# Kernel optimization log

Measured on AMD Instinct MI355X. Metric: run time of the kernel, lower is better.

The kernel has to match this reference:

```python
import jax, jax.numpy as jnp
import numpy as np
import math

B, C, H, W_ = 64, 1024, 10, 10      # C = vis_chans = ir_chans = lan_chans = m_chans
NTOK, MTOK = H * W_, 20             # 100 image tokens (W1: 100x100), 20 text tokens (W2: 100x20)
K_NN, BIG, EPS = 8, 1.0e6, 1e-8


def _minmax(t):
    # per-sample min-max normalization over the full distance slice
    mn = t.min(axis=(1, 2), keepdims=True)
    mx = t.max(axis=(1, 2), keepdims=True)
    return (t - mn) / (mx - mn + EPS)


def _geodesic(X):
    # Isomap-style geodesic distances: symmetric 8-NN Euclidean graph + Floyd-Warshall.
    P = X.shape[0]
    sq = jnp.sum(X * X, axis=-1)
    D = jnp.sqrt(jnp.maximum(sq[:, None] + sq[None, :] - 2.0 * (X @ X.T), 0.0))
    Dm = D + jnp.eye(P, dtype=X.dtype) * BIG          # exclude self from kNN
    negd, idx = jax.lax.top_k(-Dm, K_NN)              # 8 nearest neighbors per node
    A = jnp.full((P, P), BIG, X.dtype).at[jnp.arange(P)[:, None], idx].set(-negd)
    Wg = jnp.minimum(A, A.T)                          # undirected graph
    Wg = Wg.at[jnp.diag_indices(P)].set(0.0)

    def body(Dk, k):
        return jnp.minimum(Dk, Dk[:, k][:, None] + Dk[k, :][None, :]), None

    Wg, _ = jax.lax.scan(body, Wg, jnp.arange(P))
    return Wg


def _forward(ir, vis, lan, vis_w, vis_b, vis_g, vis_be, ir_w, ir_b, ir_g, ir_be,
             t_w, t_b, vout_w, vout_b, tout_w, tout_b, W1, b1, W2, b2, W4, W5,
             ml_w, ml_b, ml2_w, ml2_b, scalars):
    lam1, lam2, a1, be1, g1, a2, be2, g2, wg_aw, wg_ab, wg_bw, wg_bb = scalars
    sqc = jnp.sqrt(jnp.float32(C))
    vis_r = vis.reshape(B, C, -1).transpose(0, 2, 1)   # [B,100,C]
    ir_r = ir.reshape(B, C, -1).transpose(0, 2, 1)     # [B,100,C]
    lan_t = lan.transpose(0, 2, 1)                     # [B,20,C]

    geo = jax.vmap(_geodesic)

    # ---- compute_M_image (detached in original) ----
    joint_vi = jnp.concatenate([vis_r, ir_r], axis=1)                    # [B,200,C]
    d_vi = jax.lax.stop_gradient(geo(joint_vi))[:, :NTOK, NTOK:]         # [B,100,100]
    M_v2i_dist = _minmax(d_vi)
    sigma = jax.lax.stop_gradient(jnp.median(M_v2i_dist))
    M_v2i_fix = jnp.exp(-M_v2i_dist ** 2 / (2.0 * sigma ** 2))
    lam1s = jax.nn.sigmoid(lam1)
    M_v2i_learn = lam1s * M_v2i_fix + (1.0 - lam1s) * (W1 * M_v2i_fix + b1)

    def conv_in_relu(x, w3, b3, g3, be3, i):
        # 1x1 conv + InstanceNorm2d(affine) + ReLU, flattened to tokens
        y = jnp.einsum('bchw,mc->bmhw', x, w3[i]) + b3[i][None, :, None, None]
        mu = y.mean((2, 3), keepdims=True)
        var = y.var((2, 3), keepdims=True)
        y = (y - mu) / jnp.sqrt(var + 1e-5) * g3[i][None, :, None, None] + be3[i][None, :, None, None]
        return jax.nn.relu(y).reshape(B, C, -1).transpose(0, 2, 1)       # [B,100,C]

    Qv, Kv, Vv = [conv_in_relu(vis, vis_w, vis_b, vis_g, vis_be, i) for i in range(3)]
    Qi, Ki, Vi = [conv_in_relu(ir, ir_w, ir_b, ir_g, ir_be, i) for i in range(3)]
    Qt, Kt, Vt = [jax.nn.relu(lan_t @ t_w[i].T + t_b[i]) for i in range(3)]

    # fusion weights from GAP of the learned manifold matrix
    Mgap = M_v2i_learn.mean((1, 2), keepdims=True)       # [B,1,1]
    alpha = jax.nn.sigmoid(wg_aw * Mgap + wg_ab)
    beta = jax.nn.sigmoid(wg_bw * Mgap + wg_bb)
    Qf, Kf, Vf = alpha * Qv + beta * Qi, alpha * Kv + beta * Ki, alpha * Vv + beta * Vi
    feat_img = alpha * vis_r + beta * ir_r               # [B,100,C]

    # ---- compute_M_text (detached in original) ----
    joint_it = jnp.concatenate([feat_img, lan_t], axis=1)                # [B,120,C]
    d_it = jax.lax.stop_gradient(geo(joint_it))
    M_i2t_dist = _minmax(d_it[:, :NTOK, NTOK:])          # [B,100,20] (unused downstream, as in original)
    M_t2i_dist = _minmax(d_it[:, NTOK:, :NTOK])          # [B,20,100]
    sigma2 = jax.lax.stop_gradient(jnp.median(M_t2i_dist))
    M_t2i_fix = jnp.exp(-M_t2i_dist ** 2 / (2.0 * sigma2 ** 2))          # [B,20,100]
    M_i2t_fix = M_t2i_fix.transpose(0, 2, 1)                             # [B,100,20]
    lam2s = jax.nn.sigmoid(lam2)
    M_i2t_lo = lam2s * M_i2t_fix + (1.0 - lam2s) * (W2 * M_i2t_fix + b2) # [B,100,20]
    M_t2i_lo = M_i2t_lo.transpose(0, 2, 1)                               # [B,20,100]
    M_t2i_lo = jax.nn.softmax(M_t2i_lo / sqc, axis=2)
    M_i2t_lo = jax.nn.softmax(M_i2t_lo / sqc, axis=2)
    M_t2i_learn = (M_i2t_lo @ lan_t) @ ml_w.T + ml_b       # [B,100,C]
    M_i2t_learn = (M_t2i_lo @ feat_img) @ ml2_w.T + ml2_b  # [B,20,C]

    # ---- text->image cross attention ----
    A = Qt @ Kf.transpose(0, 2, 1) \
        + a1 * (Qt @ M_t2i_learn.transpose(0, 2, 1)) \
        + be1 * (W4 @ (M_t2i_learn @ Kf.transpose(0, 2, 1)))
    Av = jax.nn.softmax(A / sqc, axis=2)                   # [B,20,100]
    new_lan = Av @ Vf + g1 * (M_t2i_lo @ Vf)               # [B,20,C]

    # ---- image->text cross attention ----
    Bm = Qf @ Kt.transpose(0, 2, 1) \
        + a2 * (Qf @ M_i2t_learn.transpose(0, 2, 1)) \
        + be2 * (W5 @ (M_i2t_learn @ Kt.transpose(0, 2, 1)))
    Bv = jax.nn.softmax(Bm / sqc, axis=2)                  # [B,100,20]
    new_vis = Bv @ Vt + g2 * (M_i2t_lo @ Vt)               # [B,100,C]

    new_vis = new_vis.transpose(0, 2, 1).reshape(B, C, H, W_)
    new_vis = jnp.einsum('bchw,mc->bmhw', new_vis, vout_w) + vout_b[None, :, None, None]
    new_lan = new_lan @ tout_w.T + tout_b

    # ---- regularization loss ----
    fA = jax.nn.softmax(M_t2i_fix / sqc, axis=2)
    fB = jax.nn.softmax(M_i2t_fix / sqc, axis=2)
    l1 = jnp.abs(Av - fA).mean() + jnp.abs(Bv - fB).mean()
    var = lambda x: jnp.var(x, ddof=1)                    # torch .var() is unbiased
    l2 = -jnp.abs(var(Av) - var(fA)) - jnp.abs(var(Bv) - var(fB))
    loss = (l1 + 100.0 * l2) * 1000.0
    return new_vis, new_lan, loss


def setup_inputs() -> dict:
    key = jax.random.key(0)
    ks = jax.random.split(key, 20)
    f = lambda k, s, sc=1.0: jax.random.normal(k, s, jnp.float32) * sc
    return dict(
        ir=f(ks[0], (B, C, H, W_)),
        vis=f(ks[1], (B, C, H, W_)),
        lan=f(ks[2], (B, C, MTOK)),
        vis_w=f(ks[3], (3, C, C), 0.02), vis_b=jnp.zeros((3, C), jnp.float32),
        vis_g=jnp.ones((3, C), jnp.float32), vis_be=jnp.zeros((3, C), jnp.float32),
        ir_w=f(ks[4], (3, C, C), 0.02), ir_b=jnp.zeros((3, C), jnp.float32),
        ir_g=jnp.ones((3, C), jnp.float32), ir_be=jnp.zeros((3, C), jnp.float32),
        t_w=f(ks[5], (3, C, C), 0.02), t_b=jnp.zeros((3, C), jnp.float32),
        vout_w=f(ks[6], (C, C), 0.02), vout_b=jnp.zeros((C,), jnp.float32),
        tout_w=f(ks[7], (C, C), 0.02), tout_b=jnp.zeros((C,), jnp.float32),
        W1=f(ks[8], (NTOK, NTOK), 0.1), b1=jnp.zeros((NTOK, NTOK), jnp.float32),
        W2=f(ks[9], (NTOK, MTOK), 0.1), b2=jnp.zeros((NTOK, MTOK), jnp.float32),
        W4=f(ks[10], (MTOK, NTOK), 0.1),
        W5=f(ks[11], (NTOK, MTOK), 0.1),
        ml_w=f(ks[12], (C, C), 0.02), ml_b=jnp.zeros((C,), jnp.float32),
        ml2_w=f(ks[13], (C, C), 0.02), ml2_b=jnp.zeros((C,), jnp.float32),
        # [lam1, lam2, a1, b1, g1, a2, b2, g2, wg_aw, wg_ab, wg_bw, wg_bb]
        scalars=jnp.array([0.5, 0.5, 0.5, 0.5, 0.5, 0.5, 0.5, 0.5, 0.3, 0.0, 0.3, 0.0], jnp.float32),
    )


def reference(ir, vis, lan, vis_w, vis_b, vis_g, vis_be, ir_w, ir_b, ir_g, ir_be,
              t_w, t_b, vout_w, vout_b, tout_w, tout_b, W1, b1, W2, b2, W4, W5,
              ml_w, ml_b, ml2_w, ml2_b, scalars):
    return _forward(ir, vis, lan, vis_w, vis_b, vis_g, vis_be, ir_w, ir_b, ir_g, ir_be,
                    t_w, t_b, vout_w, vout_b, tout_w, tout_b, W1, b1, W2, b2, W4, W5,
                    ml_w, ml_b, ml2_w, ml2_b, scalars)
```

## Files before the change

kernel.cpp:

```cpp
#include <hip/hip_runtime.h>
#include <hip/hip_bf16.h>
#include <math.h>

#define B_   64
#define C_   1024
#define HW   100
#define MT_  20
#define P1   200
#define P2   120
#define BIGF 1.0e6f
#define EPSF 1e-8f
#define SQC  32.0f

static constexpr size_t F_J    = 0;
static constexpr size_t N_J    = (size_t)B_*P1*C_;
static constexpr size_t F_D    = F_J + N_J;
static constexpr size_t N_D    = (size_t)B_*P1*P1;
static constexpr size_t F_SQ   = F_D + N_D;
static constexpr size_t N_SQ   = (size_t)B_*P1;
static constexpr size_t F_KNN  = F_SQ + N_SQ;
static constexpr size_t N_KNN  = (size_t)B_*P1*8;
static constexpr size_t F_MV   = F_KNN + N_KNN;
static constexpr size_t N_MV   = (size_t)B_*HW*HW;
static constexpr size_t F_MT   = F_MV + N_MV;
// ... 41 lines not shown
  int c0 = blockIdx.x*32, p0 = blockIdx.y*32, b = blockIdx.z;
  int j = threadIdx.x & 31, i0 = threadIdx.x >> 5;
  for (int i = i0; i < 32; i += 8){
    int p = p0 + j;
    float v = 0.f;
    if (p < P1) v = (p < HW) ? vis[((size_t)b*C_ + c0+i)*HW + p]
                             : ir [((size_t)b*C_ + c0+i)*HW + (p-HW)];
    tile[i][j] = v;
  }
  __syncthreads();
  for (int i = i0; i < 32; i += 8){
    int p = p0 + i;
    if (p < P1) J[((size_t)b*P1 + p)*C_ + c0 + j] = tile[j][i];
  }
}

__global__ void k_pack_j2(const float* __restrict__ feat, const float* __restrict__ lan,
                          float* __restrict__ J){
  int idx = blockIdx.x*256 + threadIdx.x;
  if (idx >= B_*P2*C_) return;
  int c = idx & (C_-1);
  int p = (idx >> 10) % P2;
  int b = idx / (C_*P2);
  float v;
  if (p < HW) v = feat[((size_t)b*HW + p)*C_ + c];
  else        v = lan [((size_t)b*C_ + c)*MT_ + (p-HW)];
  J[idx] = v;
}

__global__ void k_rowsq(const float* __restrict__ J, float* __restrict__ sq, int P){
  int row = blockIdx.x;
  const float* r = J + (size_t)row*C_;
  float s = 0.f;
  for (int c = threadIdx.x; c < C_; c += 64){ float v = r[c]; s += v*v; }
  for (int o = 32; o > 0; o >>= 1) s += __shfl_down(s, o);
  if (threadIdx.x == 0) sq[row] = s;
}

__global__ __launch_bounds__(256) void k_gram_dist(const float* __restrict__ J,
    const float* __restrict__ sq, float* __restrict__ D, int P){
  __shared__ float Xi[64][33], Xj[64][33];
  int b = blockIdx.z;
  int r0 = blockIdx.x*64, s0 = blockIdx.y*64;
  int tx = threadIdx.x & 15, ty = threadIdx.x >> 4;
  const float* Jb = J + (size_t)b*P*C_;
  float acc[4][4];
  #pragma unroll
  for (int u = 0; u < 4; u++)
    #pragma unroll
    for (int v = 0; v < 4; v++) acc[u][v] = 0.f;
  for (int c0 = 0; c0 < C_; c0 += 32){
    for (int e = threadIdx.x; e < 2048; e += 256){
      int rr = e >> 5, cc = e & 31;
      Xi[rr][cc] = (r0+rr < P) ? Jb[(size_t)(r0+rr)*C_ + c0+cc] : 0.f;
      Xj[rr][cc] = (s0+rr < P) ? Jb[(size_t)(s0+rr)*C_ + c0+cc] : 0.f;
    }
    __syncthreads();
    for (int kk = 0; kk < 32; kk++){
      float xr[4], xs[4];
      #pragma unroll
      for (int u = 0; u < 4; u++) xr[u] = Xi[ty*4+u][kk];
      #pragma unroll
      for (int v = 0; v < 4; v++) xs[v] = Xj[tx*4+v][kk];
      #pragma unroll
      for (int u = 0; u < 4; u++)
        #pragma unroll
        for (int v = 0; v < 4; v++) acc[u][v] += xr[u]*xs[v];
    }
    __syncthreads();
  }
  #pragma unroll
  for (int u = 0; u < 4; u++){
    #pragma unroll
    for (int v = 0; v < 4; v++){
      int r = r0 + ty*4 + u, s = s0 + tx*4 + v;
      if (r < P && s < P){
        float d2 = sq[b*P+r] + sq[b*P+s] - 2.f*acc[u][v];
        D[((size_t)b*P + r)*P + s] = sqrtf(fmaxf(d2, 0.f));
      }
    }
  }
}

template<int P>
__global__ void k_knn(const float* __restrict__ D, int* __restrict__ knn){
  constexpr int NS = (P + 63)/64;
  int row = blockIdx.x;
  int i = row % P;
  const float* Dr = D + (size_t)row*P;
  float v[NS];
  #pragma unroll
  for (int t = 0; t < NS; t++){
    int j = threadIdx.x + t*64;
    float d = (j < P) ? Dr[j] : 4.0e6f;
    if (j == i) d += BIGF;
    v[t] = d;
  }
  for (int k = 0; k < 8; k++){
    float bv = 3.4e38f; int bj = 1 << 30;
    #pragma unroll
    for (int t = 0; t < NS; t++){
      int j = threadIdx.x + t*64;
      if (v[t] < bv){ bv = v[t]; bj = j; }
    }
    for (int o = 32; o > 0; o >>= 1){
      float ov = __shfl_xor(bv, o);
      int   oj = __shfl_xor(bj, o);
      if (ov < bv || (ov == bv && oj < bj)){ bv = ov; bj = oj; }
    }
    if (threadIdx.x == 0) knn[(size_t)row*8 + k] = bj;
    if ((bj & 63) == (int)threadIdx.x){
      #pragma unroll
      for (int t = 0; t < NS; t++) if (t == (bj >> 6)) v[t] = 3.9e38f;
    }
  }
}

__global__ void k_buildw(float* __restrict__ D, const int* __restrict__ knn, int P){
  int idx = blockIdx.x*256 + threadIdx.x;
  if (idx >= B_*P*P) return;
  int s = idx % P; int r = (idx/P) % P; int b = idx/(P*P);
  float w;
  if (r == s) w = 0.f;
  else {
    const int* ki = knn + ((size_t)b*P + r)*8;
    const int* kj = knn + ((size_t)b*P + s)*8;
    bool e = false;
    #pragma unroll
    for (int k = 0; k < 8; k++) e = e || (ki[k] == s) || (kj[k] == r);
    w = e ? D[idx] : BIGF;
  }
  D[idx] = w;
}

template<int P, int RP, int CP>
__global__ __launch_bounds__(1024) void k_fw(float* __restrict__ D){
  constexpr int PR = P/RP;
  constexpr int PC = P/CP;
  constexpr int NTH = PR*PC;
  __shared__ float rowk[P], colk[P];
  float* Db = D + (size_t)blockIdx.x*P*P;
  int tid = threadIdx.x;
  bool act = tid < NTH;
  int pi = tid / PC, pj = tid - pi*PC;
  int i0 = pi*RP, j0 = pj*CP;
  float w[RP][CP];
  if (act){
    #pragma unroll
    for (int r = 0; r < RP; r++){
      float4 v = *(const float4*)(Db + (size_t)(i0+r)*P + j0);
      w[r][0]=v.x; w[r][1]=v.y; w[r][2]=v.z; w[r][3]=v.w;
    }
  }
  for (int k = 0; k < P; k++){
    if (act){
      #pragma unroll
      for (int r = 0; r < RP; r++){
        if (i0 + r == k)
          *(float4*)(rowk + j0) = make_float4(w[r][0],w[r][1],w[r][2],w[r][3]);
      }
      #pragma unroll
      for (int c = 0; c < CP; c++){
        if (j0 + c == k){
          #pragma unroll
          for (int r = 0; r < RP; r++) colk[i0+r] = w[r][c];
        }
      }
    }
    __syncthreads();
    if (act){
      float4 rk4 = *(const float4*)(rowk + j0);
      float rk[4] = {rk4.x, rk4.y, rk4.z, rk4.w};
      float ck[RP];
      #pragma unroll
      for (int r = 0; r < RP; r++) ck[r] = colk[i0+r];
      #pragma unroll
      for (int r = 0; r < RP; r++)
        #pragma unroll
        for (int c = 0; c < CP; c++)
          w[r][c] = fminf(w[r][c], ck[r] + rk[c]);
    }
    __syncthreads();
  }
  if (act){
    #pragma unroll
    for (int r = 0; r < RP; r++)
      *(float4*)(Db + (size_t)(i0+r)*P + j0) = make_float4(w[r][0],w[r][1],w[r][2],w[r][3]);
  }
}

__global__ __launch_bounds__(256) void k_minmax(const float* __restrict__ D,
    float* __restrict__ out, int P, int r0, int c0, int R, int Cc){
  __shared__ float smn[256], smx[256];
  int b = blockIdx.x;
  const float* Db = D + (size_t)b*P*P;
  float mn = 3.4e38f, mx = -3.4e38f;
  for (int e = threadIdx.x; e < R*Cc; e += 256){
    int i = e / Cc, j = e - i*Cc;
    float v = Db[(size_t)(r0+i)*P + c0+j];
    mn = fminf(mn, v); mx = fmaxf(mx, v);
  }
  smn[threadIdx.x] = mn; smx[threadIdx.x] = mx;
  __syncthreads();
  for (int o = 128; o > 0; o >>= 1){
    if ((int)threadIdx.x < o){
      smn[threadIdx.x] = fminf(smn[threadIdx.x], smn[threadIdx.x+o]);
      smx[threadIdx.x] = fmaxf(smx[threadIdx.x], smx[threadIdx.x+o]);
    }
    __syncthreads();
  }
  mn = smn[0]; mx = smx[0];
  float inv = 1.f/(mx - mn + EPSF);
  for (int e = threadIdx.x; e < R*Cc; e += 256){
    int i = e / Cc, j = e - i*Cc;
    float v = Db[(size_t)(r0+i)*P + c0+j];
    out[((size_t)b*R + i)*Cc + j] = (v - mn)*inv;
  }
}

__global__ void k_med_init(float* hs){ if (threadIdx.x == 0){ hs[0] = 0.f; hs[1] = 1.0f; } }

__global__ __launch_bounds__(256) void k_med_hist(const float* __restrict__ x, int N,
                           const float* __restrict__ hs, unsigned* __restrict__ hist){
  __shared__ unsigned lh[1025];
  for (int i = threadIdx.x; i < 1025; i += 256) lh[i] = 0u;
  __syncthreads();
  float lo = hs[0], hi = hs[1];
  float scale = 1024.f/(hi - lo);
  unsigned below = 0;
  int idx = blockIdx.x*256 + threadIdx.x;
  int stride = gridDim.x*256;
  for (int i = idx; i < N; i += stride){
    float v = x[i];
    if (v < lo) below++;
    else if (v < hi){
      int bn = (int)((v - lo)*scale);
      if (bn > 1023) bn = 1023;
      atomicAdd(&lh[bn], 1u);
    }
  }
  for (int o = 32; o > 0; o >>= 1) below += __shfl_down(below, o);
  if ((threadIdx.x & 63) == 0 && below) atomicAdd(&lh[1024], below);
  __syncthreads();
  for (int i = threadIdx.x; i < 1025; i += 256){
    unsigned v = lh[i];
    if (v) atomicAdd(&hist[i], v);
  }
}

__global__ void k_med_select(float* hs, const unsigned* __restrict__ hist, int k){
  if (threadIdx.x != 0) return;
  float lo = hs[0], hi = hs[1], w = (hi - lo)*(1.f/1024.f);
  unsigned cum = hist[1024];
  int bf = 1023;
  for (int bn = 0; bn < 1024; bn++){
    unsigned h = hist[bn];
    if (cum + h > (unsigned)k){ bf = bn; break; }
    cum += h;
  }
  hs[0] = lo + bf*w; hs[1] = lo + (bf+1)*w;
}

__global__ __launch_bounds__(256) void k_mgap(const float* __restrict__ Mv,
    const float* __restrict__ W1, const float* __restrict__ b1,
    const float* __restrict__ sc, const float* __restrict__ hs,
    float* __restrict__ alpha, float* __restrict__ bet){
  __shared__ float sr[256];
  int b = blockIdx.x;
  float lam1s = 1.f/(1.f + expf(-sc[0]));
  float sig = 0.5f*(hs[0] + hs[1]);
  float inv2s = 1.f/(2.f*sig*sig);
  const float* Mb = Mv + (size_t)b*HW*HW;
  float s = 0.f;
  for (int e = threadIdx.x; e < HW*HW; e += 256){
    float v = Mb[e];
    float f = expf(-v*v*inv2s);
    s += lam1s*f + (1.f - lam1s)*(W1[e]*f + b1[e]);
  }
  sr[threadIdx.x] = s; __syncthreads();
  for (int o = 128; o > 0; o >>= 1){
    if ((int)threadIdx.x < o) sr[threadIdx.x] += sr[threadIdx.x+o];
    __syncthreads();
  }
  if (threadIdx.x == 0){
    float mg = sr[0]*(1.f/(HW*HW));
    alpha[b] = 1.f/(1.f + expf(-(sc[8]*mg + sc[9])));
    bet[b]   = 1.f/(1.f + expf(-(sc[10]*mg + sc[11])));
  }
}

__global__ void k_castw(const float* __restrict__ a, const float* __restrict__ b,
                        short* __restrict__ oa, short* __restrict__ ob){
  int i = (blockIdx.x*256 + threadIdx.x)*4;
  if (i >= 3*C_*C_) return;
  float4 va = *(const float4*)(a + i);
  float4 vb = *(const float4*)(b + i);
  short ra[4] = { f2bf(va.x), f2bf(va.y), f2bf(va.z), f2bf(va.w) };
  short rb[4] = { f2bf(vb.x), f2bf(vb.y), f2bf(vb.z), f2bf(vb.w) };
  *(bhalf*)(oa + i) = *(bhalf*)ra;
  *(bhalf*)(ob + i) = *(bhalf*)rb;
}

__global__ void k_cast(const float* __restrict__ a, short* __restrict__ oa, int n){
  int i = (blockIdx.x*256 + threadIdx.x)*4;
  if (i >= n) return;
  float4 va = *(const float4*)(a + i);
  short ra[4] = { f2bf(va.x), f2bf(va.y), f2bf(va.z), f2bf(va.w) };
  *(bhalf*)(oa + i) = *(bhalf*)ra;
}

__global__ __launch_bounds__(256) void k_xt2(const float* __restrict__ V,
    const float* __restrict__ I, short* __restrict__ XtV, short* __restrict__ XtI){
  __shared__ float tv[32][33], ti[32][33];
  int c0 = blockIdx.x*32, t0 = blockIdx.y*32, b = blockIdx.z;
  int j = threadIdx.x & 31, i0 = threadIdx.x >> 5;
  for (int i = i0; i < 32; i += 8){
    int t = t0 + j;
    float a = 0.f, c = 0.f;
    if (t < HW){
      a = V[((size_t)b*C_ + c0+i)*HW + t];
      c = I[((size_t)b*C_ + c0+i)*HW + t];
    }
    tv[i][j] = a; ti[i][j] = c;
  }
  __syncthreads();
  for (int i = i0; i < 32; i += 8){
    int t = t0 + i;
    if (t < HW){
      XtV[((size_t)b*HW + t)*C_ + c0 + j] = f2bf(tv[j][i]);
      XtI[((size_t)b*HW + t)*C_ + c0 + j] = f2bf(ti[j][i]);
    }
  }
}

__global__ __launch_bounds__(256) void k_lanT(const float* __restrict__ lan,
                                              short* __restrict__ lanT){
  __shared__ float tile[32][21];
  int c0 = blockIdx.x*32, b = blockIdx.y;
  for (int e = threadIdx.x; e < 32*MT_; e += 256){
    int c = e / MT_, t = e - c*MT_;
    tile[c][t] = lan[((size_t)b*C_ + c0+c)*MT_ + t];
  }
  __syncthreads();
  for (int e = threadIdx.x; e < 32*MT_; e += 256){
    int t = e >> 5, c = e & 31;
    lanT[((size_t)(b*MT_ + t))*C_ + c0 + c] = f2bf(tile[c][t]);
  }
}

__global__ __launch_bounds__(256) void k_convqkv_mfma(
    const short* __restrict__ XtV, const short* __restrict__ XtI,
    const short* __restrict__ WV,  const short* __restrict__ WI,
    const float* __restrict__ vg, const float* __restrict__ vbe,
    const float* __restrict__ ig, const float* __restrict__ ibe,
    const float* __restrict__ alpha, const float* __restrict__ bet,
    float* __restrict__ out){
  int m0 = blockIdx.x*128;
  int wsel = blockIdx.y;
  int b = blockIdx.z;
  int tid = threadIdx.x;
  int lane = tid & 63, w = tid >> 6;
  int lg = lane >> 4, lr = lane & 15;
  f32x4 acc[7][2][2];
  #pragma unroll
  for (int tf = 0; tf < 7; tf++)
    #pragma unroll
    for (int mf = 0; mf < 2; mf++)
      #pragma unroll
      for (int md = 0; md < 2; md++)
        acc[tf][mf][md] = (f32x4){0.f,0.f,0.f,0.f};
  const short* xvp = XtV + (size_t)b*HW*C_ + (size_t)lr*C_ + lg*8;
  const short* xip = XtI + (size_t)b*HW*C_ + (size_t)lr*C_ + lg*8;
  const short* wvp = WV + (size_t)wsel*C_*C_ + (size_t)(m0 + w*32 + lr)*C_ + lg*8;
  const short* wip = WI + (size_t)wsel*C_*C_ + (size_t)(m0 + w*32 + lr)*C_ + lg*8;
  const bfrag zf = {0,0,0,0,0,0,0,0};
  for (int k0 = 0; k0 < C_; k0 += 32){
    bfrag bw0v = *(const bfrag*)(wvp + k0);
    bfrag bw1v = *(const bfrag*)(wvp + (size_t)16*C_ + k0);
    bfrag bw0i = *(const bfrag*)(wip + k0);
    bfrag bw1i = *(const bfrag*)(wip + (size_t)16*C_ + k0);
    #pragma unroll
    for (int tf = 0; tf < 7; tf++){
      bfrag axv = zf, axi = zf;
      if (tf*16 + lr < HW){
        axv = *(const bfrag*)(xvp + (size_t)tf*16*C_ + k0);
        axi = *(const bfrag*)(xip + (size_t)tf*16*C_ + k0);
      }
      acc[tf][0][0] = MFMA_B16(axv, bw0v, acc[tf][0][0]);
      acc[tf][1][0] = MFMA_B16(axv, bw1v, acc[tf][1][0]);
      acc[tf][0][1] = MFMA_B16(axi, bw0i, acc[tf][0][1]);
      acc[tf][1][1] = MFMA_B16(axi, bw1i, acc[tf][1][1]);
    }
  }
  float al = alpha[b], bt = bet[b];
  float* ob = out + ((size_t)(wsel*B_ + b))*HW*C_;
  #pragma unroll
  for (int mf = 0; mf < 2; mf++){
    int m = m0 + w*32 + mf*16 + lr;
    float s1v=0.f,s2v=0.f,s1i=0.f,s2i=0.f;
    #pragma unroll
    for (int tf = 0; tf < 7; tf++){
      #pragma unroll
      for (int r = 0; r < 4; r++){
        int t = tf*16 + lg*4 + r;
        if (t < HW){
          float yv = acc[tf][mf][0][r], yi = acc[tf][mf][1][r];
          s1v += yv; s2v += yv*yv; s1i += yi; s2i += yi*yi;
        }
      }
    }
    s1v += __shfl_xor(s1v,16); s1v += __shfl_xor(s1v,32);
    s2v += __shfl_xor(s2v,16); s2v += __shfl_xor(s2v,32);
    s1i += __shfl_xor(s1i,16); s1i += __shfl_xor(s1i,32);
// ... 161 lines not shown
  }
  float* ob = out + (size_t)b*C_*HW;
  #pragma unroll
  for (int nf = 0; nf < 2; nf++){
    #pragma unroll
    for (int r = 0; r < 4; r++){
      int n = n0 + w*32 + nf*16 + lg*4 + r;
      float bv = bias[n];
      #pragma unroll
      for (int tf = 0; tf < 7; tf++){
        int t = tf*16 + lr;
        if (t < HW) ob[(size_t)n*HW + t] = acc[tf][nf][r] + bv;
      }
    }
  }
}

__global__ __launch_bounds__(256) void k_textproj_mfma(
    const short* __restrict__ lanT, const short* __restrict__ Wt,
    const float* __restrict__ tb, float* __restrict__ QKVt, float* __restrict__ lanML){
  constexpr int NROW = B_*MT_;
  __shared__ short xs[112*TPAD];
  __shared__ short wsm[128*TPAD];
  int m0 = blockIdx.x*128;
  int t0 = blockIdx.y*112;
  int wsel = blockIdx.z;
  int tid = threadIdx.x;
  int lane = tid & 63, w = tid >> 6;
  int lg = lane >> 4, lr = lane & 15;
  f32x4 acc[7][2];
  #pragma unroll
  for (int tf = 0; tf < 7; tf++)
    #pragma unroll
    for (int mf = 0; mf < 2; mf++)
      acc[tf][mf] = (f32x4){0.f,0.f,0.f,0.f};
  const short* wg = Wt + (size_t)wsel*C_*C_ + (size_t)m0*C_;
  int rr0 = tid >> 3, kk = (tid & 7)*4;
  for (int k0 = 0; k0 < C_; k0 += 32){
    __syncthreads();
    for (int rr = rr0; rr < 112; rr += 32){
      int row = t0 + rr;
      uint2 v = make_uint2(0u, 0u);
      if (row < NROW) v = *(const uint2*)(lanT + (size_t)row*C_ + k0 + kk);
      *(uint2*)&xs[rr*TPAD + kk] = v;
    }
    for (int rr = rr0; rr < 128; rr += 32)
      *(uint2*)&wsm[rr*TPAD + kk] = *(const uint2*)(wg + (size_t)rr*C_ + k0 + kk);
    __syncthreads();
    const short* pw0 = &wsm[(w*32 + lr)*TPAD + lg*4];
    const short* pw1 = &wsm[(w*32 + 16 + lr)*TPAD + lg*4];
    bhalf l0, h0;
    l0 = *(const bhalf*)pw0; h0 = *(const bhalf*)(pw0 + 16);
    bfrag bw0 = {l0[0],l0[1],l0[2],l0[3],h0[0],h0[1],h0[2],h0[3]};
    l0 = *(const bhalf*)pw1; h0 = *(const bhalf*)(pw1 + 16);
    bfrag bw1 = {l0[0],l0[1],l0[2],l0[3],h0[0],h0[1],h0[2],h0[3]};
    #pragma unroll
    for (int tf = 0; tf < 7; tf++){
      const short* pa = &xs[(tf*16 + lr)*TPAD + lg*4];
      bhalf al_ = *(const bhalf*)pa, ah_ = *(const bhalf*)(pa + 16);
      bfrag ax = {al_[0],al_[1],al_[2],al_[3],ah_[0],ah_[1],ah_[2],ah_[3]};
      acc[tf][0] = MFMA_B16(ax, bw0, acc[tf][0]);
      acc[tf][1] = MFMA_B16(ax, bw1, acc[tf][1]);
    }
  }
  bool isml = (wsel == 3);
  #pragma unroll
  for (int mf = 0; mf < 2; mf++){
    int m = m0 + w*32 + mf*16 + lr;
    float bv = isml ? 0.f : tb[wsel*C_ + m];
    #pragma unroll
    for (int tf = 0; tf < 7; tf++){
      #pragma unroll
      for (int r = 0; r < 4; r++){
        int row = t0 + tf*16 + lg*4 + r;
        if (row < NROW){
          float v = acc[tf][mf][r] + bv;
          if (!isml) v = fmaxf(v, 0.f);
          if (isml) lanML[(size_t)row*C_ + m] = v;
          else      QKVt[((size_t)wsel*NROW + row)*C_ + m] = v;
        }
      }
    }
  }
}

__global__ void k_feat(const float* __restrict__ vis, const float* __restrict__ ir,
                       const float* __restrict__ alpha, const float* __restrict__ bet,
                       float* __restrict__ feat){
  int idx = blockIdx.x*256 + threadIdx.x;
  if (idx >= B_*HW*C_) return;
  int c = idx & (C_-1);
  int t = (idx >> 10) % HW;
  int b = idx / (C_*HW);
  feat[idx] = alpha[b]*vis[((size_t)b*C_ + c)*HW + t] + bet[b]*ir[((size_t)b*C_ + c)*HW + t];
}

__global__ void k_mfixppre(const float* __restrict__ Mt, const float* __restrict__ hs2,
                           const float* __restrict__ W2, const float* __restrict__ b2,
                           const float* __restrict__ sc,
                           float* __restrict__ Mfix, float* __restrict__ Ppre){
  int idx = blockIdx.x*256 + threadIdx.x;
  if (idx >= B_*MT_*HW) return;
  int i = idx % HW;
  int j = (idx/HW) % MT_;
  int b = idx/(MT_*HW);
  float sig = 0.5f*(hs2[0] + hs2[1]);
  float v = Mt[idx];
  float f = expf(-v*v/(2.f*sig*sig));
  Mfix[idx] = f;
  float lam2s = 1.f/(1.f + expf(-sc[1]));
  Ppre[((size_t)b*HW + i)*MT_ + j] = lam2s*f + (1.f - lam2s)*(W2[i*MT_ + j]*f + b2[i*MT_ + j]);
}

__global__ __launch_bounds__(256) void k_sm20(const float* __restrict__ Ppre, float* __restrict__ Pi2t){
  int row = blockIdx.x*8 + (threadIdx.x >> 5);
  int lane = threadIdx.x & 31;
  if (row >= B_*HW) return;
  float v = (lane < MT_) ? Ppre[(size_t)row*MT_ + lane]*(1.f/SQC) : -3.4e38f;
  float m = v;
  for (int o = 16; o > 0; o >>= 1) m = fmaxf(m, __shfl_xor(m, o, 32));
  float e = (lane < MT_) ? expf(v - m) : 0.f;
  float s = e;
  for (int o = 16; o > 0; o >>= 1) s += __shfl_xor(s, o, 32);
  if (lane < MT_) Pi2t[(size_t)row*MT_ + lane] = e/s;
}

__global__ __launch_bounds__(128) void k_smT(const float* __restrict__ Ppre, float* __restrict__ Pt2i){
  __shared__ float sm[128], ss[128];
  int bj = blockIdx.x; int b = bj/MT_, j = bj % MT_;
  int i = threadIdx.x;
  float v = (i < HW) ? Ppre[((size_t)b*HW + i)*MT_ + j]*(1.f/SQC) : -3.4e38f;
  sm[i] = v; __syncthreads();
  for (int o = 64; o > 0; o >>= 1){
    if (i < o) sm[i] = fmaxf(sm[i], sm[i+o]);
    __syncthreads();
  }
  float m = sm[0];
  float e = (i < HW) ? expf(v - m) : 0.f;
  ss[i] = e; __syncthreads();
  for (int o = 64; o > 0; o >>= 1){
    if (i < o) ss[i] += ss[i+o];
    __syncthreads();
  }
  if (i < HW) Pt2i[((size_t)b*MT_ + j)*HW + i] = e/ss[0];
}

__global__ __launch_bounds__(256) void k_mlearn_t2i(const float* __restrict__ Pi2t,
    const float* __restrict__ lanML, const float* __restrict__ mlb, float* __restrict__ out){
  __shared__ float sP[HW][MT_];
  int b = blockIdx.y; int m = blockIdx.x*256 + threadIdx.x;
  for (int e = threadIdx.x; e < HW*MT_; e += 256) sP[e/MT_][e%MT_] = Pi2t[(size_t)b*HW*MT_ + e];
  __syncthreads();
  float vL[MT_];
  #pragma unroll
  for (int j = 0; j < MT_; j++) vL[j] = lanML[((size_t)b*MT_ + j)*C_ + m];
  float bb = mlb[m];
  for (int i = 0; i < HW; i++){
    float a = bb;
    #pragma unroll
    for (int j = 0; j < MT_; j++) a += sP[i][j]*vL[j];
    out[((size_t)b*HW + i)*C_ + m] = a;
  }
}

__global__ __launch_bounds__(256) void k_t2(const float* __restrict__ Pt2i,
    const float* __restrict__ feat, float* __restrict__ T2o){
  __shared__ float sP[MT_][HW];
  int b = blockIdx.y; int m = blockIdx.x*256 + threadIdx.x;
  for (int e = threadIdx.x; e < MT_*HW; e += 256) sP[e/HW][e%HW] = Pt2i[(size_t)b*MT_*HW + e];
  __syncthreads();
  float acc[MT_];
  #pragma unroll
  for (int j = 0; j < MT_; j++) acc[j] = 0.f;
  for (int i = 0; i < HW; i++){
    float f = feat[((size_t)b*HW + i)*C_ + m];
    #pragma unroll
    for (int j = 0; j < MT_; j++) acc[j] += sP[j][i]*f;
// ... 282 lines not shown
  const float* vis    = (const float*)d_in[1];
  const float* lan    = (const float*)d_in[2];
  const float* vis_w  = (const float*)d_in[3];
  const float* vis_g  = (const float*)d_in[5];
  const float* vis_be = (const float*)d_in[6];
  const float* ir_w   = (const float*)d_in[7];
  const float* ir_g   = (const float*)d_in[9];
  const float* ir_be  = (const float*)d_in[10];
  const float* t_w    = (const float*)d_in[11];
  const float* t_b    = (const float*)d_in[12];
  const float* vout_w = (const float*)d_in[13];
  const float* vout_b = (const float*)d_in[14];
  const float* tout_w = (const float*)d_in[15];
  const float* tout_b = (const float*)d_in[16];
  const float* W1     = (const float*)d_in[17];
  const float* b1     = (const float*)d_in[18];
  const float* W2     = (const float*)d_in[19];
  const float* b2     = (const float*)d_in[20];
  const float* W4     = (const float*)d_in[21];
  const float* W5     = (const float*)d_in[22];
  const float* ml_w   = (const float*)d_in[23];
  const float* ml_b   = (const float*)d_in[24];
  const float* ml2_w  = (const float*)d_in[25];
  const float* ml2_b  = (const float*)d_in[26];
  const float* sc     = (const float*)d_in[27];

  float* ws = (float*)d_ws;
  float* J     = ws + F_J;
  float* Dm    = ws + F_D;
  float* sqb   = ws + F_SQ;
  int*   knn   = (int*)(ws + F_KNN);
  float* Mv    = ws + F_MV;
  float* Mt    = ws + F_MT;
  float* Mfix  = ws + F_MFIX;
  float* QKVf  = ws + F_QKVF;
  float* QKVt  = ws + F_QKVT;
  float* feat  = ws + F_FEAT;
  float* lanML = ws + F_LANML;
  float* T2b   = ws + F_T2;
  float* Mi2tL = ws + F_MI2TL;
  float* S1    = ws + F_S1;
  float* S2    = ws + F_S2;
  float* S4a   = ws + F_S4A;
  float* S4b   = ws + F_S4B;
  float* S5    = ws + F_S5;
  float* Av    = ws + F_AV;
  float* Bv    = ws + F_BV;
  float* NL    = ws + F_NL;
  float* alpha = ws + F_AL;
  float* bet   = ws + F_BE;
  float* hs    = ws + F_HS;
  unsigned* hist = (unsigned*)(ws + F_HIST);
  float* pa    = ws + F_PA;
  float* pb    = ws + F_PB;
  float* MlT2I = ws + F_J;
  float* S3    = ws + F_D;
  float* Pi2t  = ws + F_MV;
  float* Pt2i  = ws + F_MV + 128000;
  float* Ppre  = ws + F_MV + 256000;
  short* XtV    = (short*)(ws + F_J);
  short* XtI    = (short*)(ws + F_J + 3300000);
  short* WVb    = (short*)(ws + F_J + 6600000);
  short* WIb    = (short*)(ws + F_J + 8200000);
  short* NVb    = (short*)(ws + F_J + 6553600);
  short* Wob16  = (short*)(ws + F_J + 9830400);
  short* lanTb  = (short*)(ws + F_J + 10360000);
  short* Wtb    = (short*)(ws + F_D);
  short* tout16 = (short*)(ws + F_D + 1000000);
  short* ml2w16 = (short*)(ws + F_D + 1530000);

  float* out_vis  = (float*)d_out;
  float* out_lan  = out_vis + (size_t)B_*C_*HW;
  float* out_loss = out_lan + (size_t)B_*MT_*C_;

  float* Qf = QKVf;
  float* Kf = QKVf + (size_t)B_*HW*C_;
  float* Vf = QKVf + (size_t)2*B_*HW*C_;
  float* Qt = QKVt;
  float* Kt = QKVt + (size_t)B_*MT_*C_;
  float* Vt = QKVt + (size_t)2*B_*MT_*C_;

  k_pack_j1<<<dim3(32,7,B_),256,0,stream>>>(vis, ir, J);
  k_rowsq<<<B_*P1,64,0,stream>>>(J, sqb, P1);
  k_gram_dist<<<dim3((P1+63)/64,(P1+63)/64,B_),256,0,stream>>>(J, sqb, Dm, P1);
  k_knn<P1><<<B_*P1,64,0,stream>>>(Dm, knn);
  k_buildw<<<(B_*P1*P1+255)/256,256,0,stream>>>(Dm, knn, P1);
  k_fw<P1,10,4><<<B_,1024,0,stream>>>(Dm);
  k_minmax<<<B_,256,0,stream>>>(Dm, Mv, P1, 0, 100, 100, 100);
  k_med_init<<<1,64,0,stream>>>(hs);
  for (int it = 0; it < 2; it++){
    hipMemsetAsync(hist, 0, 1025*sizeof(unsigned), stream);
    k_med_hist<<<256,256,0,stream>>>(Mv, B_*HW*HW, hs, hist);
    k_med_select<<<1,64,0,stream>>>(hs, hist, B_*HW*HW/2);
  }
  k_mgap<<<B_,256,0,stream>>>(Mv, W1, b1, sc, hs, alpha, bet);

  k_castw<<<(3*C_*C_/4+255)/256,256,0,stream>>>(vis_w, ir_w, WVb, WIb);
  k_cast<<<(C_*C_/4+255)/256,256,0,stream>>>(vout_w, Wob16, C_*C_);
  k_cast<<<(3*C_*C_/4+255)/256,256,0,stream>>>(t_w, Wtb, 3*C_*C_);
  k_cast<<<(C_*C_/4+255)/256,256,0,stream>>>(ml_w, Wtb + (size_t)3*C_*C_, C_*C_);
  k_xt2<<<dim3(32,4,B_),256,0,stream>>>(vis, ir, XtV, XtI);
  k_lanT<<<dim3(32,B_),256,0,stream>>>(lan, lanTb);
  k_convqkv_mfma<<<dim3(8,3,B_),256,0,stream>>>(XtV, XtI, WVb, WIb,
                                                vis_g, vis_be, ir_g, ir_be,
                                                alpha, bet, QKVf);
  k_textproj_mfma<<<dim3(8,12,4),256,0,stream>>>(lanTb, Wtb, t_b, QKVt, lanML);
  k_cast<<<(C_*C_/4+255)/256,256,0,stream>>>(tout_w, tout16, C_*C_);
  k_cast<<<(C_*C_/4+255)/256,256,0,stream>>>(ml2_w, ml2w16, C_*C_);
  k_feat<<<(B_*HW*C_+255)/256,256,0,stream>>>(vis, ir, alpha, bet, feat);

  k_pack_j2<<<(B_*P2*C_+255)/256,256,0,stream>>>(feat, lan, J);
  k_rowsq<<<B_*P2,64,0,stream>>>(J, sqb, P2);
  k_gram_dist<<<dim3((P2+63)/64,(P2+63)/64,B_),256,0,stream>>>(J, sqb, Dm, P2);
  k_knn<P2><<<B_*P2,64,0,stream>>>(Dm, knn);
  k_buildw<<<(B_*P2*P2+255)/256,256,0,stream>>>(Dm, knn, P2);
  k_fw<P2,4,4><<<B_,960,0,stream>>>(Dm);
  k_minmax<<<B_,256,0,stream>>>(Dm, Mt, P2, 100, 0, MT_, 100);
  k_med_init<<<1,64,0,stream>>>(hs+2);
  for (int it = 0; it < 2; it++){
    hipMemsetAsync(hist, 0, 1025*sizeof(unsigned), stream);
    k_med_hist<<<256,256,0,stream>>>(Mt, B_*MT_*HW, hs+2, hist);
    k_med_select<<<1,64,0,stream>>>(hs+2, hist, B_*MT_*HW/2);
  }
  k_mfixppre<<<(B_*MT_*HW+255)/256,256,0,stream>>>(Mt, hs+2, W2, b2, sc, Mfix, Ppre);
  k_sm20<<<(B_*HW+7)/8,256,0,stream>>>(Ppre, Pi2t);
  k_smT<<<B_*MT_,128,0,stream>>>(Ppre, Pt2i);

  k_mlearn_t2i<<<dim3(4,B_),256,0,stream>>>(Pi2t, lanML, ml_b, MlT2I);
  k_t2<<<dim3(4,B_),256,0,stream>>>(Pt2i, feat, T2b);
  k_tokproj_mfma<<<dim3(8,12),256,0,stream>>>(T2b, ml2w16, ml2_b, Mi2tL);

  k_abt2<<<dim3(2,2,B_),256,0,stream>>>(Qt, Kf, MlT2I, S1, S2, MT_, HW);
  k_s3_mfma<<<dim3(2,B_),256,0,stream>>>(MlT2I, Kf, S3);
  k_abt2<<<dim3(7,1,B_),256,0,stream>>>(Qf, Kt, Mi2tL, S4a, S4b, HW, MT_);
  k_abt<<<dim3(2,1,B_),256,0,stream>>>(Mi2tL, Kt, S5, MT_, MT_);
  k_attA<<<B_*MT_,128,0,stream>>>(S1, S2, S3, W4, sc, Av);
  k_attB<<<B_*HW/8,256,0,stream>>>(S4a, S4b, S5, W5, sc, Bv);

  k_nl<<<dim3(4,B_),256,0,stream>>>(Av, Pt2i, Vf, sc, NL);
  k_nv<<<dim3(4,B_),256,0,stream>>>(Bv, Pi2t, Vt, sc, NVb);
  k_tokproj_mfma<<<dim3(8,12),256,0,stream>>>(NL, tout16, tout_b, out_lan);
  k_convout_mfma<<<dim3(8,B_),256,0,stream>>>(NVb, Wob16, vout_b, out_vis);

  k_lossA<<<B_*MT_,128,0,stream>>>(Mfix, Av, pa);
  k_lossB<<<B_*HW/8,256,0,stream>>>(Mfix, Bv, pb);
  k_loss_final<<<1,256,0,stream>>>(pa, pb, out_loss);
}
```

Measured before the change: 2.643 ms.

## Fuse kNN graph build and min-max normalize into Floyd-Warshall; fold feat into transpose

```diff
diff --git a/kernel.cpp b/kernel.cpp
--- a/kernel.cpp
+++ b/kernel.cpp
@@ -147,6 +147,51 @@
   }
 }
 
+__global__ __launch_bounds__(256) void k_gram128(const float* __restrict__ J,
+    const float* __restrict__ sq, float* __restrict__ D, int P){
+  __shared__ float Xi[128][33], Xj[128][33];
+  int b = blockIdx.z;
+  int r0 = blockIdx.x*128, s0 = blockIdx.y*128;
+  int tx = threadIdx.x & 15, ty = threadIdx.x >> 4;
+  const float* Jb = J + (size_t)b*P*C_;
+  float acc[8][8];
+  #pragma unroll
+  for (int u = 0; u < 8; u++)
+    #pragma unroll
+    for (int v = 0; v < 8; v++) acc[u][v] = 0.f;
+  for (int c0 = 0; c0 < C_; c0 += 32){
+    for (int e = threadIdx.x; e < 4096; e += 256){
+      int rr = e >> 5, cc = e & 31;
+      Xi[rr][cc] = (r0+rr < P) ? Jb[(size_t)(r0+rr)*C_ + c0+cc] : 0.f;
+      Xj[rr][cc] = (s0+rr < P) ? Jb[(size_t)(s0+rr)*C_ + c0+cc] : 0.f;
+    }
+    __syncthreads();
+    for (int kk = 0; kk < 32; kk++){
+      float xr[8], xs[8];
+      #pragma unroll
+      for (int u = 0; u < 8; u++) xr[u] = Xi[ty*8+u][kk];
+      #pragma unroll
+      for (int v = 0; v < 8; v++) xs[v] = Xj[tx*8+v][kk];
+      #pragma unroll
+      for (int u = 0; u < 8; u++)
+        #pragma unroll
+        for (int v = 0; v < 8; v++) acc[u][v] += xr[u]*xs[v];
+    }
+    __syncthreads();
+  }
+  #pragma unroll
+  for (int u = 0; u < 8; u++){
+    #pragma unroll
+    for (int v = 0; v < 8; v++){
+      int r = r0 + ty*8 + u, s = s0 + tx*8 + v;
+      if (r < P && s < P){
+        float d2 = sq[b*P+r] + sq[b*P+s] - 2.f*acc[u][v];
+        D[((size_t)b*P + r)*P + s] = sqrtf(fmaxf(d2, 0.f));
+      }
+    }
+  }
+}
+
 template<int P>
 __global__ void k_knn(const float* __restrict__ D, int* __restrict__ knn){
   constexpr int NS = (P + 63)/64;
@@ -181,42 +226,47 @@
   }
 }
 
-__global__ void k_buildw(float* __restrict__ D, const int* __restrict__ knn, int P){
-  int idx = blockIdx.x*256 + threadIdx.x;
-  if (idx >= B_*P*P) return;
-  int s = idx % P; int r = (idx/P) % P; int b = idx/(P*P);
-  float w;
-  if (r == s) w = 0.f;
-  else {
-    const int* ki = knn + ((size_t)b*P + r)*8;
-    const int* kj = knn + ((size_t)b*P + s)*8;
-    bool e = false;
-    #pragma unroll
-    for (int k = 0; k < 8; k++) e = e || (ki[k] == s) || (kj[k] == r);
-    w = e ? D[idx] : BIGF;
-  }
-  D[idx] = w;
-}
-
-template<int P, int RP, int CP>
-__global__ __launch_bounds__(1024) void k_fw(float* __restrict__ D){
+template<int P, int NT, int RP, int CP, int R0, int C0, int RR, int CC>
+__global__ __launch_bounds__(1024) void k_fwx(const float* __restrict__ D,
+    const int* __restrict__ knn, float* __restrict__ outM){
   constexpr int PR = P/RP;
   constexpr int PC = P/CP;
   constexpr int NTH = PR*PC;
   __shared__ float rowk[P], colk[P];
-  float* Db = D + (size_t)blockIdx.x*P*P;
+  __shared__ int kl[P*8];
+  __shared__ float rmn[1024], rmx[1024];
+  int b = blockIdx.x;
+  const float* Db = D + (size_t)b*P*P;
+  const int* kb = knn + (size_t)b*P*8;
   int tid = threadIdx.x;
   bool act = tid < NTH;
   int pi = tid / PC, pj = tid - pi*PC;
   int i0 = pi*RP, j0 = pj*CP;
+  for (int e = tid; e < P*8; e += NT) kl[e] = kb[e];
+  __syncthreads();
   float w[RP][CP];
   if (act){
     #pragma unroll
     for (int r = 0; r < RP; r++){
       float4 v = *(const float4*)(Db + (size_t)(i0+r)*P + j0);
       w[r][0]=v.x; w[r][1]=v.y; w[r][2]=v.z; w[r][3]=v.w;
-    }
-  }
+      int i = i0 + r;
+      #pragma unroll
+      for (int c = 0; c < CP; c++){
+        int j = j0 + c;
+        if (i == j) w[r][c] = 0.f;
+        else {
+          const int* ki = &kl[i*8];
+          const int* kj = &kl[j*8];
+          bool e = false;
+          #pragma unroll
+          for (int k = 0; k < 8; k++) e = e || (ki[k] == j) || (kj[k] == i);
+          if (!e) w[r][c] = BIGF;
+        }
+      }
+    }
+  }
+  __syncthreads();
   for (int k = 0; k < P; k++){
     if (act){
       #pragma unroll
@@ -247,39 +297,46 @@
     }
     __syncthreads();
   }
+  float mn = 3.4e38f, mx = -3.4e38f;
   if (act){
     #pragma unroll
-    for (int r = 0; r < RP; r++)
-      *(float4*)(Db + (size_t)(i0+r)*P + j0) = make_float4(w[r][0],w[r][1],w[r][2],w[r][3]);
-  }
-}
-
-__global__ __launch_bounds__(256) void k_minmax(const float* __restrict__ D,
-    float* __restrict__ out, int P, int r0, int c0, int R, int Cc){
-  __shared__ float smn[256], smx[256];
-  int b = blockIdx.x;
-  const float* Db = D + (size_t)b*P*P;
-  float mn = 3.4e38f, mx = -3.4e38f;
-  for (int e = threadIdx.x; e < R*Cc; e += 256){
-    int i = e / Cc, j = e - i*Cc;
-    float v = Db[(size_t)(r0+i)*P + c0+j];
-    mn = fminf(mn, v); mx = fmaxf(mx, v);
-  }
-  smn[threadIdx.x] = mn; smx[threadIdx.x] = mx;
+    for (int r = 0; r < RP; r++){
+      int i = i0 + r;
+      if (i >= R0 && i < R0+RR){
+        #pragma unroll
+        for (int c = 0; c < CP; c++){
+          int j = j0 + c;
+          if (j >= C0 && j < C0+CC){
+            mn = fminf(mn, w[r][c]); mx = fmaxf(mx, w[r][c]);
+          }
+        }
+      }
+    }
+  }
+  rmn[tid] = mn; rmx[tid] = mx;
   __syncthreads();
-  for (int o = 128; o > 0; o >>= 1){
-    if ((int)threadIdx.x < o){
-      smn[threadIdx.x] = fminf(smn[threadIdx.x], smn[threadIdx.x+o]);
-      smx[threadIdx.x] = fmaxf(smx[threadIdx.x], smx[threadIdx.x+o]);
-    }
-    __syncthreads();
-  }
-  mn = smn[0]; mx = smx[0];
+  for (int o = 512; o > 0; o >>= 1){
+    if (tid < o && tid + o < NT){
+      rmn[tid] = fminf(rmn[tid], rmn[tid+o]);
+      rmx[tid] = fmaxf(rmx[tid], rmx[tid+o]);
+    }
+    __syncthreads();
+  }
+  mn = rmn[0]; mx = rmx[0];
   float inv = 1.f/(mx - mn + EPSF);
-  for (int e = threadIdx.x; e < R*Cc; e += 256){
-    int i = e / Cc, j = e - i*Cc;
-    float v = Db[(size_t)(r0+i)*P + c0+j];
-    out[((size_t)b*R + i)*Cc + j] = (v - mn)*inv;
+  if (act){
+    #pragma unroll
+    for (int r = 0; r < RP; r++){
+      int i = i0 + r;
+      if (i >= R0 && i < R0+RR){
+        #pragma unroll
+        for (int c = 0; c < CP; c++){
+          int j = j0 + c;
+          if (j >= C0 && j < C0+CC)
+            outM[((size_t)b*RR + (i-R0))*CC + (j-C0)] = (w[r][c] - mn)*inv;
+        }
+      }
+    }
   }
 }
 
@@ -375,7 +432,9 @@
 }
 
 __global__ __launch_bounds__(256) void k_xt2(const float* __restrict__ V,
-    const float* __restrict__ I, short* __restrict__ XtV, short* __restrict__ XtI){
+    const float* __restrict__ I, const float* __restrict__ alpha,
+    const float* __restrict__ bet, short* __restrict__ XtV,
+    short* __restrict__ XtI, float* __restrict__ feat){
   __shared__ float tv[32][33], ti[32][33];
   int c0 = blockIdx.x*32, t0 = blockIdx.y*32, b = blockIdx.z;
   int j = threadIdx.x & 31, i0 = threadIdx.x >> 5;
@@ -389,11 +448,15 @@
     tv[i][j] = a; ti[i][j] = c;
   }
   __syncthreads();
+  float al = alpha[b], bt = bet[b];
   for (int i = i0; i < 32; i += 8){
     int t = t0 + i;
     if (t < HW){
-      XtV[((size_t)b*HW + t)*C_ + c0 + j] = f2bf(tv[j][i]);
-      XtI[((size_t)b*HW + t)*C_ + c0 + j] = f2bf(ti[j][i]);
+      float fv = tv[j][i], fi = ti[j][i];
+      size_t off = ((size_t)b*HW + t)*C_ + c0 + j;
+      XtV[off] = f2bf(fv);
+      XtI[off] = f2bf(fi);
+      feat[off] = al*fv + bt*fi;
     }
   }
 }
@@ -721,17 +784,6 @@
       }
     }
   }
-}
-
-__global__ void k_feat(const float* __restrict__ vis, const float* __restrict__ ir,
-                       const float* __restrict__ alpha, const float* __restrict__ bet,
-                       float* __restrict__ feat){
-  int idx = blockIdx.x*256 + threadIdx.x;
-  if (idx >= B_*HW*C_) return;
-  int c = idx & (C_-1);
-  int t = (idx >> 10) % HW;
-  int b = idx / (C_*HW);
-  feat[idx] = alpha[b]*vis[((size_t)b*C_ + c)*HW + t] + bet[b]*ir[((size_t)b*C_ + c)*HW + t];
 }
 
 __global__ void k_mfixppre(const float* __restrict__ Mt, const float* __restrict__ hs2,
@@ -1180,11 +1232,9 @@
 
   k_pack_j1<<<dim3(32,7,B_),256,0,stream>>>(vis, ir, J);
   k_rowsq<<<B_*P1,64,0,stream>>>(J, sqb, P1);
-  k_gram_dist<<<dim3((P1+63)/64,(P1+63)/64,B_),256,0,stream>>>(J, sqb, Dm, P1);
+  k_gram128<<<dim3(2,2,B_),256,0,stream>>>(J, sqb, Dm, P1);
   k_knn<P1><<<B_*P1,64,0,stream>>>(Dm, knn);
-  k_buildw<<<(B_*P1*P1+255)/256,256,0,stream>>>(Dm, knn, P1);
-  k_fw<P1,10,4><<<B_,1024,0,stream>>>(Dm);
-  k_minmax<<<B_,256,0,stream>>>(Dm, Mv, P1, 0, 100, 100, 100);
+  k_fwx<P1,1024,10,4,0,100,100,100><<<B_,1024,0,stream>>>(Dm, knn, Mv);
   k_med_init<<<1,64,0,stream>>>(hs);
   for (int it = 0; it < 2; it++){
     hipMemsetAsync(hist, 0, 1025*sizeof(unsigned), stream);
@@ -1197,7 +1247,7 @@
   k_cast<<<(C_*C_/4+255)/256,256,0,stream>>>(vout_w, Wob16, C_*C_);
   k_cast<<<(3*C_*C_/4+255)/256,256,0,stream>>>(t_w, Wtb, 3*C_*C_);
   k_cast<<<(C_*C_/4+255)/256,256,0,stream>>>(ml_w, Wtb + (size_t)3*C_*C_, C_*C_);
-  k_xt2<<<dim3(32,4,B_),256,0,stream>>>(vis, ir, XtV, XtI);
+  k_xt2<<<dim3(32,4,B_),256,0,stream>>>(vis, ir, alpha, bet, XtV, XtI, feat);
   k_lanT<<<dim3(32,B_),256,0,stream>>>(lan, lanTb);
   k_convqkv_mfma<<<dim3(8,3,B_),256,0,stream>>>(XtV, XtI, WVb, WIb,
                                                 vis_g, vis_be, ir_g, ir_be,
@@ -1205,15 +1255,12 @@
   k_textproj_mfma<<<dim3(8,12,4),256,0,stream>>>(lanTb, Wtb, t_b, QKVt, lanML);
   k_cast<<<(C_*C_/4+255)/256,256,0,stream>>>(tout_w, tout16, C_*C_);
   k_cast<<<(C_*C_/4+255)/256,256,0,stream>>>(ml2_w, ml2w16, C_*C_);
-  k_feat<<<(B_*HW*C_+255)/256,256,0,stream>>>(vis, ir, alpha, bet, feat);
 
   k_pack_j2<<<(B_*P2*C_+255)/256,256,0,stream>>>(feat, lan, J);
   k_rowsq<<<B_*P2,64,0,stream>>>(J, sqb, P2);
-  k_gram_dist<<<dim3((P2+63)/64,(P2+63)/64,B_),256,0,stream>>>(J, sqb, Dm, P2);
+  k_gram_dist<<<dim3(2,2,B_),256,0,stream>>>(J, sqb, Dm, P2);
   k_knn<P2><<<B_*P2,64,0,stream>>>(Dm, knn);
-  k_buildw<<<(B_*P2*P2+255)/256,256,0,stream>>>(Dm, knn, P2);
-  k_fw<P2,4,4><<<B_,960,0,stream>>>(Dm);
-  k_minmax<<<B_,256,0,stream>>>(Dm, Mt, P2, 100, 0, MT_, 100);
+  k_fwx<P2,960,4,4,100,0,MT_,100><<<B_,960,0,stream>>>(Dm, knn, Mt);
   k_med_init<<<1,64,0,stream>>>(hs+2);
   for (int it = 0; it < 2; it++){
     hipMemsetAsync(hist, 0, 1025*sizeof(unsigned), stream);
```

Measured after the change: 2.825 ms. 1.07x slower.
